# Kernel tuning notes

Hardware: AMD Instinct MI355X
Metric: run time of the kernel (lower is better)

The kernel has to match this reference:

```python
import jax, jax.numpy as jnp
import numpy as np

B = 524288
EPS = 1e-4  # ReEig clamp


def setup_inputs() -> dict:
    key = jax.random.key(0)
    kx, k1, k2, k3 = jax.random.split(key, 4)
    A = jax.random.normal(kx, (B, 9, 9), dtype=jnp.float32)
    # batch of SPD matrices: A A^T / 9 + small ridge
    X = jnp.einsum('bik,bjk->bij', A, A) / 9.0 + 1e-3 * jnp.eye(9, dtype=jnp.float32)
    W1 = jnp.linalg.qr(jax.random.normal(k1, (9, 7), dtype=jnp.float32))[0]
    W2 = jnp.linalg.qr(jax.random.normal(k2, (7, 5), dtype=jnp.float32))[0]
    W3 = jnp.linalg.qr(jax.random.normal(k3, (5, 3), dtype=jnp.float32))[0]
    return {"X": X, "W1": W1, "W2": W2, "W3": W3}


def _bimap(X, W):
    # W^T X W, batched: out[b,a,c] = sum_ij W[i,a] X[b,i,j] W[j,c]
    return jnp.einsum('ia,bij,jc->bac', W, X, W)


def _reeig(X):
    w, v = jnp.linalg.eigh(X)
    w = jnp.maximum(w, EPS)
    return jnp.einsum('bik,bk,bjk->bij', v, w, v)


def _logeig(X):
    w, v = jnp.linalg.eigh(X)
    return jnp.einsum('bik,bk,bjk->bij', v, jnp.log(w), v)


def reference(X, W1, W2, W3):
    C = _reeig(_bimap(X, W1))   # [B,7,7]
    C = _reeig(_bimap(C, W2))   # [B,5,5]
    C = _reeig(_bimap(C, W3))   # [B,3,3]
    C = _logeig(C)              # [B,3,3]
    i, j = jnp.triu_indices(3)  # upper-triangle vech, 6 entries
    return C[:, i, j]           # [B,6]
```

## Files before the change

### kernel.cpp

```cpp
#include <hip/hip_runtime.h>
#include <math.h>
#include <stdint.h>


#define GLOBAL_AS __attribute__((address_space(1)))
#define LDS_AS    __attribute__((address_space(3)))

__device__ __forceinline__ float fast_rcp(float x)  { return __builtin_amdgcn_rcpf(x); }
__device__ __forceinline__ float fast_rsq(float x)  { return __builtin_amdgcn_rsqf(x); }
__device__ __forceinline__ float fast_sqrt(float x) { return __builtin_amdgcn_sqrtf(x); }
__device__ __forceinline__ float fast_log(float x)  { return __builtin_amdgcn_logf(x) * 0.69314718056f; }

#define JACOBI_ROT(app, aqq, apq, arp, arq, vp0, vq0, vp1, vq1, vp2, vq2)      \
  do {                                                                         \
    float _apq = apq;                                                          \
    float _tau = (aqq - app) * 0.5f * fast_rcp(_apq);                          \
    float _t = copysignf(fast_rcp(fabsf(_tau) + fast_sqrt(fmaf(_tau, _tau, 1.f))), _tau); \
    _t = (fabsf(_apq) > 1e-20f) ? _t : 0.f;                                    \
    float _c = fast_rsq(fmaf(_t, _t, 1.f));                                    \
    float _s = _t * _c;                                                        \
    float _arp = arp, _arq = arq;                                              \
    arp = _c * _arp - _s * _arq;                                               \
    arq = _s * _arp + _c * _arq;                                               \
    app = fmaf(-_t, _apq, app);                                                \
    aqq = fmaf(_t, _apq, aqq);                                                 \
    apq = 0.f;                                                                 \
    float _v;                                                                  \
    _v = vp0; vp0 = _c * _v - _s * vq0; vq0 = _s * _v + _c * vq0;              \
    _v = vp1; vp1 = _c * _v - _s * vq1; vq1 = _s * _v + _c * vq1;              \
    _v = vp2; vp2 = _c * _v - _s * vq2; vq2 = _s * _v + _c * vq2;              \
  } while (0)

__global__ __launch_bounds__(64) void spd_encoder_kernel(
    const float* __restrict__ X,
    const float* __restrict__ W1,
    const float* __restrict__ W2,
    const float* __restrict__ W3,
    float* __restrict__ out)
{
    __shared__ float sX[5184];
    __shared__ float sM[27];

    const int lane = threadIdx.x;
    const long long base = (long long)blockIdx.x * 64;

    {
        GLOBAL_AS const float* g = (GLOBAL_AS const float*)(X + base * 81);
        #pragma unroll
        for (int k = 0; k < 20; ++k)
            __builtin_amdgcn_global_load_lds(
                (GLOBAL_AS const void*)(g + k * 256 + lane * 4),
                (LDS_AS void*)(sX + k * 256), 16, 0, 0);
        __builtin_amdgcn_global_load_lds(
            (GLOBAL_AS const void*)(g + 5120 + lane),
            (LDS_AS void*)(sX + 5120), 4, 0, 0);
    }

    if (lane < 27) {
        const int i = lane / 3, c = lane % 3;
        float acc = 0.f;
        #pragma unroll
        for (int a = 0; a < 7; ++a) {
            float p = 0.f;
            #pragma unroll
            for (int b = 0; b < 5; ++b)
                p = fmaf(W2[a * 5 + b], W3[b * 3 + c], p);
            acc = fmaf(W1[i * 7 + a], p, acc);
        }
        sM[lane] = acc;
    }

    __syncthreads();

    float M[9][3];
    #pragma unroll
    for (int i = 0; i < 9; ++i)
        #pragma unroll
        for (int c = 0; c < 3; ++c)
            M[i][c] = sM[i * 3 + c];

    const float* __restrict__ x = sX + lane * 81;
    float T[9][3];
    #pragma unroll
    for (int i = 0; i < 9; ++i) {
        float t0 = 0.f, t1 = 0.f, t2 = 0.f;
        #pragma unroll
        for (int j = 0; j < 9; ++j) {
            const float xv = x[i * 9 + j];
            t0 = fmaf(xv, M[j][0], t0);
            t1 = fmaf(xv, M[j][1], t1);
            t2 = fmaf(xv, M[j][2], t2);
        }
        T[i][0] = t0; T[i][1] = t1; T[i][2] = t2;
    }

    float A00 = 0.f, A01 = 0.f, A02 = 0.f, A11 = 0.f, A12 = 0.f, A22 = 0.f;
    #pragma unroll
    for (int i = 0; i < 9; ++i) {
        A00 = fmaf(M[i][0], T[i][0], A00);
        A01 = fmaf(M[i][0], T[i][1], A01);
        A02 = fmaf(M[i][0], T[i][2], A02);
        A11 = fmaf(M[i][1], T[i][1], A11);
        A12 = fmaf(M[i][1], T[i][2], A12);
        A22 = fmaf(M[i][2], T[i][2], A22);
    }

    float V00 = 1.f, V01 = 0.f, V02 = 0.f;
    float V10 = 0.f, V11 = 1.f, V12 = 0.f;
    float V20 = 0.f, V21 = 0.f, V22 = 1.f;

    #pragma unroll
    for (int sw = 0; sw < 5; ++sw) {
        JACOBI_ROT(A00, A11, A01, A02, A12, V00, V01, V10, V11, V20, V21);
        JACOBI_ROT(A00, A22, A02, A01, A12, V00, V02, V10, V12, V20, V22);
        JACOBI_ROT(A11, A22, A12, A01, A02, V01, V02, V11, V12, V21, V22);
    }

    const float lw0 = fast_log(fmaxf(A00, 1e-12f));
    const float lw1 = fast_log(fmaxf(A11, 1e-12f));
    const float lw2 = fast_log(fmaxf(A22, 1e-12f));

    const float L00 = lw0 * V00 * V00 + lw1 * V01 * V01 + lw2 * V02 * V02;
    const float L01 = lw0 * V00 * V10 + lw1 * V01 * V11 + lw2 * V02 * V12;
    const float L02 = lw0 * V00 * V20 + lw1 * V01 * V21 + lw2 * V02 * V22;
    const float L11 = lw0 * V10 * V10 + lw1 * V11 * V11 + lw2 * V12 * V12;
    const float L12 = lw0 * V10 * V20 + lw1 * V11 * V21 + lw2 * V12 * V22;
    const float L22 = lw0 * V20 * V20 + lw1 * V21 * V21 + lw2 * V22 * V22;

    float2* o2 = (float2*)(out + (base + lane) * 6);
    o2[0] = make_float2(L00, L01);
    o2[1] = make_float2(L02, L11);
    o2[2] = make_float2(L12, L22);
}

extern "C" void kernel_launch(void* const* d_in, const int* in_sizes, int n_in,
                              void* d_out, int out_size, void* d_ws, size_t ws_size,
                              hipStream_t stream) {
    const float* X  = (const float*)d_in[0];
    const float* W1 = (const float*)d_in[1];
    const float* W2 = (const float*)d_in[2];
    const float* W3 = (const float*)d_in[3];
    float* out = (float*)d_out;

    const int B = in_sizes[0] / 81;
    const int nblocks = B / 64;
    spd_encoder_kernel<<<nblocks, 64, 0, stream>>>(X, W1, W2, W3, out);
}
```

Baseline: 239.1 us.

## Make encoder kernel persistent with double-buffered LDS tile prefetch

The kernel now launches a fixed grid of 768 single-wave blocks that stride over all 64-matrix tiles, instead of one block per tile. Each block keeps two LDS buffers and issues the asynchronous global-to-LDS load for the next tile before computing the current one. A manual vmcnt wait holds back only until the current tile has landed. The goal is to hide load latency behind the Jacobi eigen-solve and to pay the fused weight-matrix setup once per block. In exchange, only a few waves are resident per CU, LDS use per block doubles, and the last iteration redundantly reloads its own tile.

```diff
diff --git a/kernel.cpp b/kernel.cpp
--- a/kernel.cpp
+++ b/kernel.cpp
@@ -31,30 +31,32 @@
     _v = vp2; vp2 = _c * _v - _s * vq2; vq2 = _s * _v + _c * vq2;              \
   } while (0)
 
+__device__ __forceinline__ void issue_tile(const float* __restrict__ X,
+                                           long long tile, float* dst, int lane)
+{
+    GLOBAL_AS const float* g = (GLOBAL_AS const float*)(X + tile * 5184);
+    #pragma unroll
+    for (int k = 0; k < 20; ++k)
+        __builtin_amdgcn_global_load_lds(
+            (GLOBAL_AS const void*)(g + k * 256 + lane * 4),
+            (LDS_AS void*)(dst + k * 256), 16, 0, 0);
+    __builtin_amdgcn_global_load_lds(
+        (GLOBAL_AS const void*)(g + 5120 + lane),
+        (LDS_AS void*)(dst + 5120), 4, 0, 0);
+}
+
 __global__ __launch_bounds__(64) void spd_encoder_kernel(
     const float* __restrict__ X,
     const float* __restrict__ W1,
     const float* __restrict__ W2,
     const float* __restrict__ W3,
-    float* __restrict__ out)
+    float* __restrict__ out,
+    int ntiles)
 {
-    __shared__ float sX[5184];
+    __shared__ float sX[2][5184];
     __shared__ float sM[27];
 
     const int lane = threadIdx.x;
-    const long long base = (long long)blockIdx.x * 64;
-
-    {
-        GLOBAL_AS const float* g = (GLOBAL_AS const float*)(X + base * 81);
-        #pragma unroll
-        for (int k = 0; k < 20; ++k)
-            __builtin_amdgcn_global_load_lds(
-                (GLOBAL_AS const void*)(g + k * 256 + lane * 4),
-                (LDS_AS void*)(sX + k * 256), 16, 0, 0);
-        __builtin_amdgcn_global_load_lds(
-            (GLOBAL_AS const void*)(g + 5120 + lane),
-            (LDS_AS void*)(sX + 5120), 4, 0, 0);
-    }
 
     if (lane < 27) {
         const int i = lane / 3, c = lane % 3;
@@ -69,7 +71,6 @@
         }
         sM[lane] = acc;
     }
-
     __syncthreads();
 
     float M[9][3];
@@ -79,58 +80,74 @@
         for (int c = 0; c < 3; ++c)
             M[i][c] = sM[i * 3 + c];
 
-    const float* __restrict__ x = sX + lane * 81;
-    float T[9][3];
-    #pragma unroll
-    for (int i = 0; i < 9; ++i) {
-        float t0 = 0.f, t1 = 0.f, t2 = 0.f;
+    const int stride = gridDim.x;
+    long long t = blockIdx.x;
+    if (t >= ntiles) return;
+
+    issue_tile(X, t, &sX[0][0], lane);
+    int buf = 0;
+
+    for (; t < ntiles; t += stride) {
+        long long nt = t + stride;
+        if (nt >= ntiles) nt = t;
+        issue_tile(X, nt, &sX[buf ^ 1][0], lane);
+
+        asm volatile("s_waitcnt vmcnt(21)" ::: "memory");
+
+        const float* __restrict__ x = &sX[buf][0] + lane * 81;
+        float T[9][3];
         #pragma unroll
-        for (int j = 0; j < 9; ++j) {
-            const float xv = x[i * 9 + j];
-            t0 = fmaf(xv, M[j][0], t0);
-            t1 = fmaf(xv, M[j][1], t1);
-            t2 = fmaf(xv, M[j][2], t2);
+        for (int i = 0; i < 9; ++i) {
+            float t0 = 0.f, t1 = 0.f, t2 = 0.f;
+            #pragma unroll
+            for (int j = 0; j < 9; ++j) {
+                const float xv = x[i * 9 + j];
+                t0 = fmaf(xv, M[j][0], t0);
+                t1 = fmaf(xv, M[j][1], t1);
+                t2 = fmaf(xv, M[j][2], t2);
+            }
+            T[i][0] = t0; T[i][1] = t1; T[i][2] = t2;
         }
-        T[i][0] = t0; T[i][1] = t1; T[i][2] = t2;
+
+        float A00 = 0.f, A01 = 0.f, A02 = 0.f, A11 = 0.f, A12 = 0.f, A22 = 0.f;
+        #pragma unroll
+        for (int i = 0; i < 9; ++i) {
+            A00 = fmaf(M[i][0], T[i][0], A00);
+            A01 = fmaf(M[i][0], T[i][1], A01);
+            A02 = fmaf(M[i][0], T[i][2], A02);
+            A11 = fmaf(M[i][1], T[i][1], A11);
+            A12 = fmaf(M[i][1], T[i][2], A12);
+            A22 = fmaf(M[i][2], T[i][2], A22);
+        }
+
+        float V00 = 1.f, V01 = 0.f, V02 = 0.f;
+        float V10 = 0.f, V11 = 1.f, V12 = 0.f;
+        float V20 = 0.f, V21 = 0.f, V22 = 1.f;
+        #pragma unroll
+        for (int sw = 0; sw < 5; ++sw) {
+            JACOBI_ROT(A00, A11, A01, A02, A12, V00, V01, V10, V11, V20, V21);
+            JACOBI_ROT(A00, A22, A02, A01, A12, V00, V02, V10, V12, V20, V22);
+            JACOBI_ROT(A11, A22, A12, A01, A02, V01, V02, V11, V12, V21, V22);
+        }
+
+        const float lw0 = fast_log(fmaxf(A00, 1e-12f));
+        const float lw1 = fast_log(fmaxf(A11, 1e-12f));
+        const float lw2 = fast_log(fmaxf(A22, 1e-12f));
+
+        const float L00 = lw0 * V00 * V00 + lw1 * V01 * V01 + lw2 * V02 * V02;
+        const float L01 = lw0 * V00 * V10 + lw1 * V01 * V11 + lw2 * V02 * V12;
+        const float L02 = lw0 * V00 * V20 + lw1 * V01 * V21 + lw2 * V02 * V22;
+        const float L11 = lw0 * V10 * V10 + lw1 * V11 * V11 + lw2 * V12 * V12;
+        const float L12 = lw0 * V10 * V20 + lw1 * V11 * V21 + lw2 * V12 * V22;
+        const float L22 = lw0 * V20 * V20 + lw1 * V21 * V21 + lw2 * V22 * V22;
+
+        float2* o2 = (float2*)(out + (t * 64 + lane) * 6);
+        o2[0] = make_float2(L00, L01);
+        o2[1] = make_float2(L02, L11);
+        o2[2] = make_float2(L12, L22);
+
+        buf ^= 1;
     }
-
-    float A00 = 0.f, A01 = 0.f, A02 = 0.f, A11 = 0.f, A12 = 0.f, A22 = 0.f;
-    #pragma unroll
-    for (int i = 0; i < 9; ++i) {
-        A00 = fmaf(M[i][0], T[i][0], A00);
-        A01 = fmaf(M[i][0], T[i][1], A01);
-        A02 = fmaf(M[i][0], T[i][2], A02);
-        A11 = fmaf(M[i][1], T[i][1], A11);
-        A12 = fmaf(M[i][1], T[i][2], A12);
-        A22 = fmaf(M[i][2], T[i][2], A22);
-    }
-
-    float V00 = 1.f, V01 = 0.f, V02 = 0.f;
-    float V10 = 0.f, V11 = 1.f, V12 = 0.f;
-    float V20 = 0.f, V21 = 0.f, V22 = 1.f;
-
-    #pragma unroll
-    for (int sw = 0; sw < 5; ++sw) {
-        JACOBI_ROT(A00, A11, A01, A02, A12, V00, V01, V10, V11, V20, V21);
-        JACOBI_ROT(A00, A22, A02, A01, A12, V00, V02, V10, V12, V20, V22);
-        JACOBI_ROT(A11, A22, A12, A01, A02, V01, V02, V11, V12, V21, V22);
-    }
-
-    const float lw0 = fast_log(fmaxf(A00, 1e-12f));
-    const float lw1 = fast_log(fmaxf(A11, 1e-12f));
-    const float lw2 = fast_log(fmaxf(A22, 1e-12f));
-
-    const float L00 = lw0 * V00 * V00 + lw1 * V01 * V01 + lw2 * V02 * V02;
-    const float L01 = lw0 * V00 * V10 + lw1 * V01 * V11 + lw2 * V02 * V12;
-    const float L02 = lw0 * V00 * V20 + lw1 * V01 * V21 + lw2 * V02 * V22;
-    const float L11 = lw0 * V10 * V10 + lw1 * V11 * V11 + lw2 * V12 * V12;
-    const float L12 = lw0 * V10 * V20 + lw1 * V11 * V21 + lw2 * V12 * V22;
-    const float L22 = lw0 * V20 * V20 + lw1 * V21 * V21 + lw2 * V22 * V22;
-
-    float2* o2 = (float2*)(out + (base + lane) * 6);
-    o2[0] = make_float2(L00, L01);
-    o2[1] = make_float2(L02, L11);
-    o2[2] = make_float2(L12, L22);
 }
 
 extern "C" void kernel_launch(void* const* d_in, const int* in_sizes, int n_in,
@@ -143,6 +160,7 @@
     float* out = (float*)d_out;
 
     const int B = in_sizes[0] / 81;
-    const int nblocks = B / 64;
-    spd_encoder_kernel<<<nblocks, 64, 0, stream>>>(X, W1, W2, W3, out);
+    const int ntiles = B / 64;
+    const int nblocks = 768;
+    spd_encoder_kernel<<<nblocks, 64, 0, stream>>>(X, W1, W2, W3, out, ntiles);
 }
```

After: 249.3 us. +4.2%, slower.
